# Performance work log

Hardware: AMD Instinct MI355X
Metric: run time of the kernel (lower is better)

The kernel has to match this reference:

```python
import jax, jax.numpy as jnp
import numpy as np

N_QUESTIONS = 2000
N_CATS = 4
MEMORY_SIZE = 50
KEY_DIM = 50
VALUE_DIM = 200
FINAL_FC = 50
ABILITY_SCALE = 3.0
BATCH = 1024
SEQ_LEN = 500


def setup_inputs() -> dict:
    key = jax.random.key(0)
    ks = jax.random.split(key, 20)
    f32 = jnp.float32
    inp = {}
    # integer data: question ids in [1, n_questions], responses in [0, K)
    inp['q_data'] = jax.random.randint(ks[0], (BATCH, SEQ_LEN), 1, N_QUESTIONS + 1)
    inp['r_data'] = jax.random.randint(ks[1], (BATCH, SEQ_LEN), 0, N_CATS)
    s = 0.05
    inp['q_embed_w'] = jax.random.normal(ks[2], (N_QUESTIONS + 1, KEY_DIM), f32) * s
    inp['Mk'] = jax.random.normal(ks[3], (MEMORY_SIZE, KEY_DIM), f32) * s
    inp['Mv0'] = jax.random.normal(ks[4], (MEMORY_SIZE, VALUE_DIM), f32) * s
    inp['Wv'] = jax.random.normal(ks[5], (VALUE_DIM, N_CATS * N_QUESTIONS), f32) * s
    inp['bv'] = jnp.zeros((VALUE_DIM,), f32)
    # DKVMN erase / add transforms
    inp['We'] = jax.random.normal(ks[6], (VALUE_DIM, VALUE_DIM), f32) * s
    inp['be'] = jnp.zeros((VALUE_DIM,), f32)
    inp['Wa'] = jax.random.normal(ks[7], (VALUE_DIM, VALUE_DIM), f32) * s
    inp['ba'] = jnp.zeros((VALUE_DIM,), f32)
    # summary network
    inp['Ws'] = jax.random.normal(ks[8], (FINAL_FC, VALUE_DIM + KEY_DIM), f32) * s
    inp['bs'] = jnp.zeros((FINAL_FC,), f32)
    # ability / threshold / discrimination heads
    inp['Wth'] = jax.random.normal(ks[9], (1, FINAL_FC), f32) * s
    inp['bth'] = jnp.zeros((1,), f32)
    inp['Wbeta'] = jax.random.normal(ks[10], (N_CATS - 1, KEY_DIM), f32) * s
    inp['bbeta'] = jnp.zeros((N_CATS - 1,), f32)
    inp['Wdisc'] = jax.random.normal(ks[11], (1, FINAL_FC + KEY_DIM), f32) * s
    inp['bdisc'] = jnp.zeros((1,), f32)
    return inp


def _deep_gpcm(q_data, r_data, q_embed_w, Mk, Mv0, Wv, bv, We, be, Wa, ba,
               Ws, bs, Wth, bth, Wbeta, bbeta, Wdisc, bdisc):
    B, S = q_data.shape
    K = Wbeta.shape[0] + 1
    D = Wv.shape[0]
    Q = Wv.shape[1] // K
    # view gpcm_value_embed weight as (D, K, Q): one-hot(q) @ W == gather column q
    WvK = Wv.reshape(D, K, Q)
    k_idx = jnp.arange(K, dtype=jnp.float32)
    Mv_init = jnp.broadcast_to(Mv0[None], (B,) + Mv0.shape)

    def step(Mv, inp):
        q_t, r_t = inp  # (B,), (B,)
        qe = q_embed_w[q_t]  # (B, key_dim)
        # linear decay weights: max(0, 1 - |k - r| / (K-1))
        w = jnp.maximum(0.0, 1.0 - jnp.abs(k_idx[None, :] - r_t[:, None].astype(jnp.float32)) / (K - 1))  # (B, K)
        Wvq = jnp.take(WvK, q_t - 1, axis=2)  # (D, K, B)
        ve = jnp.einsum('dkb,bk->bd', Wvq, w) + bv  # value embedding (B, D)
        # DKVMN attention + read
        cw = jax.nn.softmax(qe @ Mk.T, axis=-1)  # (B, mem)
        read = jnp.einsum('bm,bmd->bd', cw, Mv)
        # summary / IRT heads
        summary = jnp.tanh(jnp.concatenate([read, qe], axis=-1) @ Ws.T + bs)  # (B, fc)
        theta = ABILITY_SCALE * (summary @ Wth.T + bth)[:, 0]  # (B,)
        betas = jnp.tanh(qe @ Wbeta.T + bbeta)  # (B, K-1)
        alpha = jax.nn.softplus(jnp.concatenate([summary, qe], axis=-1) @ Wdisc.T + bdisc)[:, 0]  # (B,)
        # erase-add memory write
        erase = jax.nn.sigmoid(ve @ We.T + be)
        add = jnp.tanh(ve @ Wa.T + ba)
        Mv_new = Mv * (1.0 - cw[:, :, None] * erase[:, None, :]) + cw[:, :, None] * add[:, None, :]
        # GPCM cumulative logits -> softmax
        cum = jnp.cumsum(alpha[:, None] * (theta[:, None] - betas), axis=-1)  # (B, K-1)
        logits = jnp.concatenate([jnp.zeros((B, 1), cum.dtype), cum], axis=-1)  # (B, K)
        probs = jax.nn.softmax(logits, axis=-1)
        return Mv_new, probs

    _, probs = jax.lax.scan(step, Mv_init, (q_data.T, r_data.T))  # (S, B, K)
    return jnp.transpose(probs, (1, 0, 2))  # (B, S, K)


def reference(q_data, r_data, q_embed_w, Mk, Mv0, Wv, bv, We, be, Wa, ba,
              Ws, bs, Wth, bth, Wbeta, bbeta, Wdisc, bdisc):
    return _deep_gpcm(q_data, r_data, q_embed_w, Mk, Mv0, Wv, bv, We, be, Wa, ba,
                      Ws, bs, Wth, bth, Wbeta, bbeta, Wdisc, bdisc)
```

## Files before the change

kernel.cpp:

```cpp
#include <hip/hip_runtime.h>
#include <hip/hip_bf16.h>
#include <cstdint>
#include <cstddef>


namespace {
constexpr int kB   = 1024;
constexpr int kS   = 500;
constexpr int kQ   = 2000;
constexpr int kKD  = 50;
constexpr int kMem = 50;
constexpr int kD   = 200;
constexpr int kFC  = 50;
constexpr int kWP  = 216;

constexpr size_t OFF_EAD  = 0;
constexpr size_t OFF_CW   = OFF_EAD + (size_t)kQ * 4 * kD * 2;
constexpr size_t OFF_SQ   = OFF_CW + 100064;
constexpr size_t OFF_BQ   = OFF_SQ + 100064;
constexpr size_t OFF_DQ   = OFF_BQ + 8032;
constexpr size_t OFF_CE   = OFF_DQ + 2016;
constexpr size_t OFF_CA   = OFF_CE + 224;
constexpr size_t OFF_WET  = OFF_CA + 224;
constexpr size_t OFF_WAT  = OFF_WET + 40000;
}

typedef float f32x2 __attribute__((ext_vector_type(2)));
typedef _Float16 h2_t __attribute__((ext_vector_type(2)));

__device__ __forceinline__ f32x2 pk_fma(f32x2 a, f32x2 b, f32x2 c) {
  f32x2 d;
  asm("v_pk_fma_f32 %0, %1, %2, %3" : "=v"(d) : "v"(a), "v"(b), "v"(c));
  return d;
}

__device__ __forceinline__ void lds_barrier() {
  asm volatile("s_waitcnt lgkmcnt(0)" ::: "memory");
  __builtin_amdgcn_s_barrier();
  asm volatile("" ::: "memory");
}

__device__ __forceinline__ float fast_tanh(float x) {
  const float ax = fabsf(x);
  const float t = __expf(-2.f * ax);
  const float r = (1.f - t) / (1.f + t);
  return copysignf(r, x);
}
__device__ __forceinline__ float fast_softplus(float x) {
  return fmaxf(x, 0.f) + log1pf(__expf(-fabsf(x)));
}

__global__ void prep1_misc(const float* __restrict__ We, const float* __restrict__ Wa,
                           const float* __restrict__ bv, const float* __restrict__ be,
                           const float* __restrict__ ba, float* __restrict__ ws) {
  float* WeT = ws + OFF_WET;
  float* WaT = ws + OFF_WAT;
  float* ce  = ws + OFF_CE;
  float* ca  = ws + OFF_CA;
  const int gt = blockIdx.x * 256 + threadIdx.x;
  const int stride = gridDim.x * 256;
  for (int e = gt; e < kD * kD; e += stride) {
    const int i = e / kD;
    const int dd = e - i * kD;
    WeT[e] = We[dd * kD + i];
    WaT[e] = Wa[dd * kD + i];
  }
  for (int dd = gt; dd < kD; dd += stride) {
    float acc_e = be[dd], acc_a = ba[dd];
    for (int i = 0; i < kD; ++i) {
      acc_e = fmaf(We[dd * kD + i], bv[i], acc_e);
      acc_a = fmaf(Wa[dd * kD + i], bv[i], acc_a);
    }
    ce[dd] = acc_e;
    ca[dd] = acc_a;
  }
}

__global__ void prep2_ead(const float* __restrict__ Wv, float* __restrict__ ws) {
  __shared__ float s_wv[4][kD];
  const int tid = threadIdx.x;
  const int qm1 = blockIdx.x;
  for (int e = tid; e < 4 * kD; e += 256) {
    const int k = e / kD;
    const int i = e - k * kD;
    s_wv[k][i] = Wv[(size_t)i * (4 * kQ) + (size_t)k * kQ + qm1];
  }
  __syncthreads();
  const int d = tid;
  if (d < kD) {
    const float* WeT = ws + OFF_WET;
    const float* WaT = ws + OFF_WAT;
    float e0 = 0.f, e1 = 0.f, e2 = 0.f, e3 = 0.f;
    float a0 = 0.f, a1 = 0.f, a2 = 0.f, a3 = 0.f;
    for (int i = 0; i < kD; ++i) {
      const float we = WeT[i * kD + d];
      const float wa = WaT[i * kD + d];
      e0 = fmaf(we, s_wv[0][i], e0);
      e1 = fmaf(we, s_wv[1][i], e1);
      e2 = fmaf(we, s_wv[2][i], e2);
      e3 = fmaf(we, s_wv[3][i], e3);
      a0 = fmaf(wa, s_wv[0][i], a0);
      a1 = fmaf(wa, s_wv[1][i], a1);
      a2 = fmaf(wa, s_wv[2][i], a2);
      a3 = fmaf(wa, s_wv[3][i], a3);
    }
    const float ced = ws[OFF_CE + d];
    const float cad = ws[OFF_CA + d];
    const float W[4][4] = {{1.f, 2.f / 3.f, 1.f / 3.f, 0.f},
                           {2.f / 3.f, 1.f, 2.f / 3.f, 1.f / 3.f},
                           {1.f / 3.f, 2.f / 3.f, 1.f, 2.f / 3.f},
                           {0.f, 1.f / 3.f, 2.f / 3.f, 1.f}};
#pragma unroll
    for (int r = 0; r < 4; ++r) {
      const float ep = ced + W[r][0] * e0 + W[r][1] * e1 + W[r][2] * e2 + W[r][3] * e3;
      const float ap = cad + W[r][0] * a0 + W[r][1] * a1 + W[r][2] * a2 + W[r][3] * a3;
      float2 v;
      v.x = 1.f / (1.f + expf(-ep));
      v.y = tanhf(ap);
      *reinterpret_cast<float2*>(ws + OFF_EAD + ((size_t)(qm1 * 4 + r) * kD + d) * 2) = v;
    }
  }
}

__global__ void prep3_qtables(const float* __restrict__ q_embed_w, const float* __restrict__ Mk,
                              const float* __restrict__ Ws, const float* __restrict__ bs,
                              const float* __restrict__ Wbeta, const float* __restrict__ bbeta,
                              const float* __restrict__ Wdisc, float* __restrict__ ws) {
  __shared__ float s_qe[kKD];
  const int tid = threadIdx.x;
  const int q = blockIdx.x;
  if (tid < kKD) s_qe[tid] = q_embed_w[q * kKD + tid];
  __syncthreads();
  {
    float s = -1e30f;
    if (tid < kMem) {
      s = 0.f;
      for (int j = 0; j < kKD; ++j) s = fmaf(s_qe[j], Mk[tid * kKD + j], s);
    }
    float mx = s;
#pragma unroll
    for (int o = 1; o < 64; o <<= 1) mx = fmaxf(mx, __shfl_xor(mx, o));
    const float ev = (tid < kMem) ? expf(s - mx) : 0.f;
    float sm = ev;
#pragma unroll
    for (int o = 1; o < 64; o <<= 1) sm += __shfl_xor(sm, o);
    if (tid < kMem) ws[OFF_CW + (size_t)q * kMem + tid] = ev / sm;
  }
  if (tid < kFC) {
    float s = bs[tid];
    for (int j = 0; j < kKD; ++j) s = fmaf(s_qe[j], Ws[tid * 250 + kD + j], s);
    ws[OFF_SQ + (size_t)q * kFC + tid] = s;
  }
  if (tid < 4) {
    float v = 0.f;
    if (tid < 3) {
      float s = bbeta[tid];
      for (int j = 0; j < kKD; ++j) s = fmaf(s_qe[j], Wbeta[tid * kKD + j], s);
      v = tanhf(s);
    }
    ws[OFF_BQ + (size_t)q * 4 + tid] = v;
  }
  if (tid == 0) {
    float s = 0.f;
    for (int j = 0; j < kKD; ++j) s = fmaf(s_qe[j], Wdisc[kFC + j], s);
    ws[OFF_DQ + q] = s;
  }
}

__device__ __forceinline__ void do_finale(int l, float wth_f, float wds_f, float bth0,
                                          float bdisc0, const float (*s_part)[64],
                                          const float* s_sq_row, const float* s_bqdq_row,
                                          float* out_ptr) {
  float summ = 0.f;
  if (l < kFC) {
    const float sp = s_part[0][l] + s_part[1][l] + s_part[2][l] + s_part[3][l] +
                     s_part[4][l] + s_sq_row[l];
    summ = fast_tanh(sp);
  }
  float p1 = wth_f * summ;
  float p2 = wds_f * summ;
#pragma unroll
  for (int o = 1; o < 64; o <<= 1) {
    p1 += __shfl_xor(p1, o);
    p2 += __shfl_xor(p2, o);
  }
  if (l == 0) {
    const float theta = 3.f * (p1 + bth0);
    const float alpha = fast_softplus(p2 + s_bqdq_row[3] + bdisc0);
    const float c1 = alpha * (theta - s_bqdq_row[0]);
    const float c2 = c1 + alpha * (theta - s_bqdq_row[1]);
    const float c3 = c2 + alpha * (theta - s_bqdq_row[2]);
    const float mx = fmaxf(fmaxf(0.f, c1), fmaxf(c2, c3));
    const float x0 = __expf(0.f - mx);
    const float x1 = __expf(c1 - mx);
    const float x2 = __expf(c2 - mx);
    const float x3 = __expf(c3 - mx);
    const float inv = 1.f / (x0 + x1 + x2 + x3);
    float4 pr;
    pr.x = x0 * inv;
    pr.y = x1 * inv;
    pr.z = x2 * inv;
    pr.w = x3 * inv;
    *reinterpret_cast<float4*>(out_ptr) = pr;
  }
}

__launch_bounds__(256, 4)
__global__ void dkvmn_main(const int* __restrict__ q_data, const int* __restrict__ r_data,
                           const float* __restrict__ Mv0, const float* __restrict__ Ws,
                           const float* __restrict__ Wth, const float* __restrict__ bth,
                           const float* __restrict__ Wdisc, const float* __restrict__ bdisc,
                           const float* __restrict__ ws, float* __restrict__ out) {
  const int tid = threadIdx.x;
  const int b = blockIdx.x;
  const int lane = tid & 63;
  const int wid = tid >> 6;
  const float* EAD = ws + OFF_EAD;
  const float* CW = ws + OFF_CW;
  const float* SQ = ws + OFF_SQ;
  const float* BQ = ws + OFF_BQ;
  const float* DQ = ws + OFF_DQ;

  __shared__ __align__(16) _Float16 s_wsh[kFC * kWP];
  __shared__ __align__(16) _Float16 s_readh[2][208];
  __shared__ __align__(16) float s_cw[2][64];
  __shared__ float s_part[2][5][64];
  __shared__ float s_sq[3][52];
  __shared__ float s_bqdq[3][4];
  __shared__ int s_q[kS];
  __shared__ int s_qr[kS];

  for (int e = tid; e < kFC * kD; e += 256) {
    const int f = e / kD;
    const int dd = e - f * kD;
    s_wsh[f * kWP + dd] = (_Float16)Ws[f * 250 + dd];
  }
  {
    const int* qrow = q_data + (size_t)b * kS;
    const int* rrow = r_data + (size_t)b * kS;
    for (int e = tid; e < kS; e += 256) {
      const int qv = qrow[e];
      s_q[e] = qv;
      s_qr[e] = (qv - 1) * 4 + rrow[e];
    }
  }
  f32x2 mv[25];
  const int d = tid;
  const bool dact = (d < kD);
  if (dact) {
#pragma unroll
    for (int m = 0; m < 25; ++m) {
      mv[m][0] = Mv0[(2 * m) * kD + d];
      mv[m][1] = Mv0[(2 * m + 1) * kD + d];
    }
  }
  float wth_f = 0.f, wds_f = 0.f;
  if (wid == 3 && lane < kFC) {
    wth_f = Wth[lane];
    wds_f = Wdisc[lane];
  }
  const float bth0 = bth[0];
  const float bdisc0 = bdisc[0];
  float* out_b = out + (size_t)b * kS * 4;
  __syncthreads();

  const int q0 = s_q[0];
  const int q1 = s_q[1];
  float2 ea_cur = make_float2(0.f, 0.f);
  if (dact) ea_cur = *reinterpret_cast<const float2*>(EAD + ((size_t)s_qr[0] * kD + d) * 2);
  float cw_cur = 0.f;
  if (wid == 1 && lane < kMem) {
    s_cw[0][lane] = CW[(size_t)q0 * kMem + lane];
    cw_cur = CW[(size_t)q1 * kMem + lane];
  }
  float v2_cur = 0.f;
  if (wid == 2) {
    if (lane < kFC) v2_cur = SQ[(size_t)q0 * kFC + lane];
    else if (lane < 53) v2_cur = BQ[(size_t)q0 * 4 + (lane - 50)];
    else if (lane == 53) v2_cur = DQ[q0];
  }
  __syncthreads();

  int i3 = 0;
  for (int t = 0; t < kS; ++t) {
    const int pb = t & 1;
    const int ip1 = (i3 + 1 < 3) ? i3 + 1 : 0;
    const int tn1 = (t + 1 < kS) ? t + 1 : kS - 1;
    const int tn2 = (t + 2 < kS) ? t + 2 : kS - 1;
    f32x2 en2 = {0.f, 0.f}, ad2 = {0.f, 0.f};
    float2 ea_nxt = ea_cur;
    if (dact) {
      ea_nxt = *reinterpret_cast<const float2*>(EAD + ((size_t)s_qr[tn1] * kD + d) * 2);
      en2[0] = -ea_cur.x;
      en2[1] = -ea_cur.x;
      ad2[0] = ea_cur.y;
      ad2[1] = ea_cur.y;
    }
    if (wid == 1 && lane < kMem) {
      s_cw[pb ^ 1][lane] = cw_cur;
      cw_cur = CW[(size_t)s_q[tn2] * kMem + lane];
    }
    if (wid == 2) {
      const int qn = s_q[tn1];
      if (lane < kFC) {
        s_sq[i3][lane] = v2_cur;
        v2_cur = SQ[(size_t)qn * kFC + lane];
      } else if (lane < 53) {
        s_bqdq[i3][lane - 50] = v2_cur;
        v2_cur = BQ[(size_t)qn * 4 + (lane - 50)];
      } else if (lane == 53) {
        s_bqdq[i3][3] = v2_cur;
        v2_cur = DQ[qn];
      }
    }
    if (dact) {
      f32x2 r2a = {0.f, 0.f}, r2b = {0.f, 0.f};
      const float4* cw4 = reinterpret_cast<const float4*>(s_cw[pb]);
#pragma unroll
      for (int g = 0; g < 12; ++g) {
        const float4 c4 = cw4[g];
        const f32x2 clo = {c4.x, c4.y};
        const f32x2 chi = {c4.z, c4.w};
        r2a = pk_fma(clo, mv[2 * g], r2a);
        mv[2 * g] = pk_fma(clo, pk_fma(mv[2 * g], en2, ad2), mv[2 * g]);
        r2b = pk_fma(chi, mv[2 * g + 1], r2b);
        mv[2 * g + 1] = pk_fma(chi, pk_fma(mv[2 * g + 1], en2, ad2), mv[2 * g + 1]);
      }
      {
        const f32x2 clast = *reinterpret_cast<const f32x2*>(&s_cw[pb][48]);
        r2a = pk_fma(clast, mv[24], r2a);
        mv[24] = pk_fma(clast, pk_fma(mv[24], en2, ad2), mv[24]);
      }
      s_readh[pb][d] = (_Float16)((r2a[0] + r2b[0]) + (r2a[1] + r2b[1]));
    }
    if (wid == 3 && t >= 2) {
      do_finale(lane, wth_f, wds_f, bth0, bdisc0, s_part[pb ^ 1], s_sq[ip1], s_bqdq[ip1],
                out_b + (size_t)(t - 2) * 4);
    }
    if (tid < 250) {
      const int pc = tid / 50;
      const int pf = tid - pc * 50;
      const float4* wp = reinterpret_cast<const float4*>(s_wsh + pf * kWP + pc * 40);
      const float4* rp = reinterpret_cast<const float4*>(&s_readh[pb ^ 1][pc * 40]);
      float acc0 = 0.f, acc1 = 0.f;
#pragma unroll
      for (int g = 0; g < 5; ++g) {
        const float4 wv = wp[g];
        const float4 rv = rp[g];
        acc0 = __builtin_amdgcn_fdot2(__builtin_bit_cast(h2_t, wv.x),
                                      __builtin_bit_cast(h2_t, rv.x), acc0, false);
        acc1 = __builtin_amdgcn_fdot2(__builtin_bit_cast(h2_t, wv.y),
                                      __builtin_bit_cast(h2_t, rv.y), acc1, false);
        acc0 = __builtin_amdgcn_fdot2(__builtin_bit_cast(h2_t, wv.z),
                                      __builtin_bit_cast(h2_t, rv.z), acc0, false);
        acc1 = __builtin_amdgcn_fdot2(__builtin_bit_cast(h2_t, wv.w),
                                      __builtin_bit_cast(h2_t, rv.w), acc1, false);
      }
      s_part[pb][pc][pf] = acc0 + acc1;
    }
    lds_barrier();
    ea_cur = ea_nxt;
    i3 = ip1;
  }
  {
    constexpr int pbE = kS & 1;
    constexpr int i3a = (kS - 2) % 3;
    constexpr int i3b = (kS - 1) % 3;
    if (tid < 250) {
      const int pc = tid / 50;
      const int pf = tid - pc * 50;
      const float4* wp = reinterpret_cast<const float4*>(s_wsh + pf * kWP + pc * 40);
      const float4* rp = reinterpret_cast<const float4*>(&s_readh[(kS - 1) & 1][pc * 40]);
      float acc0 = 0.f, acc1 = 0.f;
#pragma unroll
      for (int g = 0; g < 5; ++g) {
        const float4 wv = wp[g];
        const float4 rv = rp[g];
        acc0 = __builtin_amdgcn_fdot2(__builtin_bit_cast(h2_t, wv.x),
                                      __builtin_bit_cast(h2_t, rv.x), acc0, false);
        acc1 = __builtin_amdgcn_fdot2(__builtin_bit_cast(h2_t, wv.y),
                                      __builtin_bit_cast(h2_t, rv.y), acc1, false);
        acc0 = __builtin_amdgcn_fdot2(__builtin_bit_cast(h2_t, wv.z),
                                      __builtin_bit_cast(h2_t, rv.z), acc0, false);
        acc1 = __builtin_amdgcn_fdot2(__builtin_bit_cast(h2_t, wv.w),
                                      __builtin_bit_cast(h2_t, rv.w), acc1, false);
      }
      s_part[pbE][pc][pf] = acc0 + acc1;
    }
    if (wid == 3) {
      do_finale(lane, wth_f, wds_f, bth0, bdisc0, s_part[pbE ^ 1], s_sq[i3a], s_bqdq[i3a],
                out_b + (size_t)(kS - 2) * 4);
    }
    lds_barrier();
    if (wid == 3) {
      do_finale(lane, wth_f, wds_f, bth0, bdisc0, s_part[pbE], s_sq[i3b], s_bqdq[i3b],
                out_b + (size_t)(kS - 1) * 4);
    }
  }
}

extern "C" void kernel_launch(void* const* d_in, const int* in_sizes, int n_in,
                              void* d_out, int out_size, void* d_ws, size_t ws_size,
                              hipStream_t stream) {
  (void)in_sizes; (void)n_in; (void)out_size; (void)ws_size;
  const int* q_data = (const int*)d_in[0];
  const int* r_data = (const int*)d_in[1];
  const float* q_embed_w = (const float*)d_in[2];
  const float* Mk = (const float*)d_in[3];
  const float* Mv0 = (const float*)d_in[4];
  const float* Wv = (const float*)d_in[5];
  const float* bv = (const float*)d_in[6];
  const float* We = (const float*)d_in[7];
  const float* be = (const float*)d_in[8];
  const float* Wa = (const float*)d_in[9];
  const float* ba = (const float*)d_in[10];
  const float* Ws = (const float*)d_in[11];
  const float* bs = (const float*)d_in[12];
  const float* Wth = (const float*)d_in[13];
  const float* bth = (const float*)d_in[14];
  const float* Wbeta = (const float*)d_in[15];
  const float* bbeta = (const float*)d_in[16];
  const float* Wdisc = (const float*)d_in[17];
  const float* bdisc = (const float*)d_in[18];
  float* out = (float*)d_out;
  float* ws = (float*)d_ws;

  hipLaunchKernelGGL(prep1_misc, dim3(64), dim3(256), 0, stream, We, Wa, bv, be, ba, ws);
  hipLaunchKernelGGL(prep2_ead, dim3(kQ), dim3(256), 0, stream, Wv, ws);
  hipLaunchKernelGGL(prep3_qtables, dim3(kQ + 1), dim3(64), 0, stream, q_embed_w, Mk, Ws, bs,
                     Wbeta, bbeta, Wdisc, ws);
  hipLaunchKernelGGL(dkvmn_main, dim3(kB), dim3(256), 0, stream, q_data, r_data, Mv0, Ws, Wth,
                     bth, Wdisc, bdisc, ws, out);
}
```

Baseline: 1.246 ms.

## Split memory-slot update across two threads per value column with 512-thread blocks

Doubles the block to 512 threads. The 50 memory slots of each value column are now split between two threads, which halves the per-thread serial FMA chain and the register footprint of the memory state. Load and finale roles move to warps 0 and 1. The Ws dot-product threads now add the two partial read vectors in fp16 before the fdot2. This adds thread-level parallelism in the sequential scan step, at the cost of an extra fp16 add (with some precision loss) and larger barrier groups.

```diff
diff --git a/kernel.cpp b/kernel.cpp
--- a/kernel.cpp
+++ b/kernel.cpp
@@ -205,7 +205,7 @@
   }
 }
 
-__launch_bounds__(256, 4)
+__launch_bounds__(512, 8)
 __global__ void dkvmn_main(const int* __restrict__ q_data, const int* __restrict__ r_data,
                            const float* __restrict__ Mv0, const float* __restrict__ Ws,
                            const float* __restrict__ Wth, const float* __restrict__ bth,
@@ -222,7 +222,7 @@
   const float* DQ = ws + OFF_DQ;
 
   __shared__ __align__(16) _Float16 s_wsh[kFC * kWP];
-  __shared__ __align__(16) _Float16 s_readh[2][208];
+  __shared__ __align__(16) _Float16 s_readh[2][2][208];
   __shared__ __align__(16) float s_cw[2][64];
   __shared__ float s_part[2][5][64];
   __shared__ float s_sq[3][52];
@@ -230,7 +230,7 @@
   __shared__ int s_q[kS];
   __shared__ int s_qr[kS];
 
-  for (int e = tid; e < kFC * kD; e += 256) {
+  for (int e = tid; e < kFC * kD; e += 512) {
     const int f = e / kD;
     const int dd = e - f * kD;
     s_wsh[f * kWP + dd] = (_Float16)Ws[f * 250 + dd];
@@ -238,24 +238,40 @@
   {
     const int* qrow = q_data + (size_t)b * kS;
     const int* rrow = r_data + (size_t)b * kS;
-    for (int e = tid; e < kS; e += 256) {
+    for (int e = tid; e < kS; e += 512) {
       const int qv = qrow[e];
       s_q[e] = qv;
       s_qr[e] = (qv - 1) * 4 + rrow[e];
     }
   }
-  f32x2 mv[25];
-  const int d = tid;
-  const bool dact = (d < kD);
+  const bool dact = (tid >= 112);
+  const int u = tid - 112;
+  const bool half1 = (u >= 200);
+  const int d = half1 ? (u - 200) : u;
+  const int p0 = half1 ? 13 : 0;
+
+  const bool pact = (tid >= 262);
+  const int pidx = tid - 262;
+  const int pc = pidx / 50;
+  const int pf = pidx - pc * 50;
+
+  f32x2 mv[13];
+#pragma unroll
+  for (int j = 0; j < 13; ++j) mv[j] = f32x2{0.f, 0.f};
   if (dact) {
 #pragma unroll
-    for (int m = 0; m < 25; ++m) {
-      mv[m][0] = Mv0[(2 * m) * kD + d];
-      mv[m][1] = Mv0[(2 * m + 1) * kD + d];
+    for (int j = 0; j < 12; ++j) {
+      const int m2 = 2 * (p0 + j);
+      mv[j][0] = Mv0[m2 * kD + d];
+      mv[j][1] = Mv0[(m2 + 1) * kD + d];
+    }
+    if (!half1) {
+      mv[12][0] = Mv0[24 * kD + d];
+      mv[12][1] = Mv0[25 * kD + d];
     }
   }
   float wth_f = 0.f, wds_f = 0.f;
-  if (wid == 3 && lane < kFC) {
+  if (wid == 0 && lane < kFC) {
     wth_f = Wth[lane];
     wds_f = Wdisc[lane];
   }
@@ -267,16 +283,16 @@
   const int q0 = s_q[0];
   const int q1 = s_q[1];
   float2 ea_cur = make_float2(0.f, 0.f);
-  if (dact) ea_cur = *reinterpret_cast<const float2*>(EAD + ((size_t)s_qr[0] * kD + d) * 2);
+  if (dact) ea_cur = *(reinterpret_cast<const float2*>(EAD) + (s_qr[0] * kD + d));
   float cw_cur = 0.f;
-  if (wid == 1 && lane < kMem) {
-    s_cw[0][lane] = CW[(size_t)q0 * kMem + lane];
-    cw_cur = CW[(size_t)q1 * kMem + lane];
+  if (wid == 0 && lane < kMem) {
+    s_cw[0][lane] = CW[q0 * kMem + lane];
+    cw_cur = CW[q1 * kMem + lane];
   }
   float v2_cur = 0.f;
-  if (wid == 2) {
-    if (lane < kFC) v2_cur = SQ[(size_t)q0 * kFC + lane];
-    else if (lane < 53) v2_cur = BQ[(size_t)q0 * 4 + (lane - 50)];
+  if (wid == 1) {
+    if (lane < kFC) v2_cur = SQ[q0 * kFC + lane];
+    else if (lane < 53) v2_cur = BQ[q0 * 4 + (lane - 50)];
     else if (lane == 53) v2_cur = DQ[q0];
   }
   __syncthreads();
@@ -290,24 +306,24 @@
     f32x2 en2 = {0.f, 0.f}, ad2 = {0.f, 0.f};
     float2 ea_nxt = ea_cur;
     if (dact) {
-      ea_nxt = *reinterpret_cast<const float2*>(EAD + ((size_t)s_qr[tn1] * kD + d) * 2);
+      ea_nxt = *(reinterpret_cast<const float2*>(EAD) + (s_qr[tn1] * kD + d));
       en2[0] = -ea_cur.x;
       en2[1] = -ea_cur.x;
       ad2[0] = ea_cur.y;
       ad2[1] = ea_cur.y;
     }
-    if (wid == 1 && lane < kMem) {
+    if (wid == 0 && lane < kMem) {
       s_cw[pb ^ 1][lane] = cw_cur;
-      cw_cur = CW[(size_t)s_q[tn2] * kMem + lane];
-    }
-    if (wid == 2) {
+      cw_cur = CW[s_q[tn2] * kMem + lane];
+    }
+    if (wid == 1) {
       const int qn = s_q[tn1];
       if (lane < kFC) {
         s_sq[i3][lane] = v2_cur;
-        v2_cur = SQ[(size_t)qn * kFC + lane];
+        v2_cur = SQ[qn * kFC + lane];
       } else if (lane < 53) {
         s_bqdq[i3][lane - 50] = v2_cur;
-        v2_cur = BQ[(size_t)qn * 4 + (lane - 50)];
+        v2_cur = BQ[qn * 4 + (lane - 50)];
       } else if (lane == 53) {
         s_bqdq[i3][3] = v2_cur;
         v2_cur = DQ[qn];
@@ -315,46 +331,46 @@
     }
     if (dact) {
       f32x2 r2a = {0.f, 0.f}, r2b = {0.f, 0.f};
-      const float4* cw4 = reinterpret_cast<const float4*>(s_cw[pb]);
-#pragma unroll
-      for (int g = 0; g < 12; ++g) {
-        const float4 c4 = cw4[g];
-        const f32x2 clo = {c4.x, c4.y};
-        const f32x2 chi = {c4.z, c4.w};
-        r2a = pk_fma(clo, mv[2 * g], r2a);
-        mv[2 * g] = pk_fma(clo, pk_fma(mv[2 * g], en2, ad2), mv[2 * g]);
-        r2b = pk_fma(chi, mv[2 * g + 1], r2b);
-        mv[2 * g + 1] = pk_fma(chi, pk_fma(mv[2 * g + 1], en2, ad2), mv[2 * g + 1]);
+      const f32x2* cw2 = reinterpret_cast<const f32x2*>(s_cw[pb]) + p0;
+#pragma unroll
+      for (int j = 0; j < 12; ++j) {
+        const f32x2 c2 = cw2[j];
+        if (j & 1) {
+          r2b = pk_fma(c2, mv[j], r2b);
+        } else {
+          r2a = pk_fma(c2, mv[j], r2a);
+        }
+        mv[j] = pk_fma(c2, pk_fma(mv[j], en2, ad2), mv[j]);
       }
-      {
-        const f32x2 clast = *reinterpret_cast<const f32x2*>(&s_cw[pb][48]);
-        r2a = pk_fma(clast, mv[24], r2a);
-        mv[24] = pk_fma(clast, pk_fma(mv[24], en2, ad2), mv[24]);
+      if (!half1) {
+        const f32x2 c2 = cw2[12];
+        r2a = pk_fma(c2, mv[12], r2a);
+        mv[12] = pk_fma(c2, pk_fma(mv[12], en2, ad2), mv[12]);
       }
-      s_readh[pb][d] = (_Float16)((r2a[0] + r2b[0]) + (r2a[1] + r2b[1]));
-    }
-    if (wid == 3 && t >= 2) {
+      s_readh[pb][half1][d] = (_Float16)((r2a[0] + r2b[0]) + (r2a[1] + r2b[1]));
+    }
+    if (wid == 0 && t >= 2) {
       do_finale(lane, wth_f, wds_f, bth0, bdisc0, s_part[pb ^ 1], s_sq[ip1], s_bqdq[ip1],
                 out_b + (size_t)(t - 2) * 4);
     }
-    if (tid < 250) {
-      const int pc = tid / 50;
-      const int pf = tid - pc * 50;
+    if (pact) {
       const float4* wp = reinterpret_cast<const float4*>(s_wsh + pf * kWP + pc * 40);
-      const float4* rp = reinterpret_cast<const float4*>(&s_readh[pb ^ 1][pc * 40]);
+      const float4* rpA = reinterpret_cast<const float4*>(&s_readh[pb ^ 1][0][pc * 40]);
+      const float4* rpB = reinterpret_cast<const float4*>(&s_readh[pb ^ 1][1][pc * 40]);
       float acc0 = 0.f, acc1 = 0.f;
 #pragma unroll
       for (int g = 0; g < 5; ++g) {
         const float4 wv = wp[g];
-        const float4 rv = rp[g];
-        acc0 = __builtin_amdgcn_fdot2(__builtin_bit_cast(h2_t, wv.x),
-                                      __builtin_bit_cast(h2_t, rv.x), acc0, false);
-        acc1 = __builtin_amdgcn_fdot2(__builtin_bit_cast(h2_t, wv.y),
-                                      __builtin_bit_cast(h2_t, rv.y), acc1, false);
-        acc0 = __builtin_amdgcn_fdot2(__builtin_bit_cast(h2_t, wv.z),
-                                      __builtin_bit_cast(h2_t, rv.z), acc0, false);
-        acc1 = __builtin_amdgcn_fdot2(__builtin_bit_cast(h2_t, wv.w),
-                                      __builtin_bit_cast(h2_t, rv.w), acc1, false);
+        const float4 va = rpA[g];
+        const float4 vb = rpB[g];
+        const h2_t r0 = __builtin_bit_cast(h2_t, va.x) + __builtin_bit_cast(h2_t, vb.x);
+        const h2_t r1 = __builtin_bit_cast(h2_t, va.y) + __builtin_bit_cast(h2_t, vb.y);
+        const h2_t r2 = __builtin_bit_cast(h2_t, va.z) + __builtin_bit_cast(h2_t, vb.z);
+        const h2_t r3 = __builtin_bit_cast(h2_t, va.w) + __builtin_bit_cast(h2_t, vb.w);
+        acc0 = __builtin_amdgcn_fdot2(__builtin_bit_cast(h2_t, wv.x), r0, acc0, false);
+        acc1 = __builtin_amdgcn_fdot2(__builtin_bit_cast(h2_t, wv.y), r1, acc1, false);
+        acc0 = __builtin_amdgcn_fdot2(__builtin_bit_cast(h2_t, wv.z), r2, acc0, false);
+        acc1 = __builtin_amdgcn_fdot2(__builtin_bit_cast(h2_t, wv.w), r3, acc1, false);
       }
       s_part[pb][pc][pf] = acc0 + acc1;
     }
@@ -366,33 +382,33 @@
     constexpr int pbE = kS & 1;
     constexpr int i3a = (kS - 2) % 3;
     constexpr int i3b = (kS - 1) % 3;
-    if (tid < 250) {
-      const int pc = tid / 50;
-      const int pf = tid - pc * 50;
+    if (pact) {
       const float4* wp = reinterpret_cast<const float4*>(s_wsh + pf * kWP + pc * 40);
-      const float4* rp = reinterpret_cast<const float4*>(&s_readh[(kS - 1) & 1][pc * 40]);
+      const float4* rpA = reinterpret_cast<const float4*>(&s_readh[(kS - 1) & 1][0][pc * 40]);
+      const float4* rpB = reinterpret_cast<const float4*>(&s_readh[(kS - 1) & 1][1][pc * 40]);
       float acc0 = 0.f, acc1 = 0.f;
 #pragma unroll
       for (int g = 0; g < 5; ++g) {
         const float4 wv = wp[g];
-        const float4 rv = rp[g];
-        acc0 = __builtin_amdgcn_fdot2(__builtin_bit_cast(h2_t, wv.x),
-                                      __builtin_bit_cast(h2_t, rv.x), acc0, false);
-        acc1 = __builtin_amdgcn_fdot2(__builtin_bit_cast(h2_t, wv.y),
-                                      __builtin_bit_cast(h2_t, rv.y), acc1, false);
-        acc0 = __builtin_amdgcn_fdot2(__builtin_bit_cast(h2_t, wv.z),
-                                      __builtin_bit_cast(h2_t, rv.z), acc0, false);
-        acc1 = __builtin_amdgcn_fdot2(__builtin_bit_cast(h2_t, wv.w),
-                                      __builtin_bit_cast(h2_t, rv.w), acc1, false);
+        const float4 va = rpA[g];
+        const float4 vb = rpB[g];
+        const h2_t r0 = __builtin_bit_cast(h2_t, va.x) + __builtin_bit_cast(h2_t, vb.x);
+        const h2_t r1 = __builtin_bit_cast(h2_t, va.y) + __builtin_bit_cast(h2_t, vb.y);
+        const h2_t r2 = __builtin_bit_cast(h2_t, va.z) + __builtin_bit_cast(h2_t, vb.z);
+        const h2_t r3 = __builtin_bit_cast(h2_t, va.w) + __builtin_bit_cast(h2_t, vb.w);
+        acc0 = __builtin_amdgcn_fdot2(__builtin_bit_cast(h2_t, wv.x), r0, acc0, false);
+        acc1 = __builtin_amdgcn_fdot2(__builtin_bit_cast(h2_t, wv.y), r1, acc1, false);
+        acc0 = __builtin_amdgcn_fdot2(__builtin_bit_cast(h2_t, wv.z), r2, acc0, false);
+        acc1 = __builtin_amdgcn_fdot2(__builtin_bit_cast(h2_t, wv.w), r3, acc1, false);
       }
       s_part[pbE][pc][pf] = acc0 + acc1;
     }
-    if (wid == 3) {
+    if (wid == 0) {
       do_finale(lane, wth_f, wds_f, bth0, bdisc0, s_part[pbE ^ 1], s_sq[i3a], s_bqdq[i3a],
                 out_b + (size_t)(kS - 2) * 4);
     }
     lds_barrier();
-    if (wid == 3) {
+    if (wid == 0) {
       do_finale(lane, wth_f, wds_f, bth0, bdisc0, s_part[pbE], s_sq[i3b], s_bqdq[i3b],
                 out_b + (size_t)(kS - 1) * 4);
     }
@@ -429,6 +445,6 @@
   hipLaunchKernelGGL(prep2_ead, dim3(kQ), dim3(256), 0, stream, Wv, ws);
   hipLaunchKernelGGL(prep3_qtables, dim3(kQ + 1), dim3(64), 0, stream, q_embed_w, Mk, Ws, bs,
                      Wbeta, bbeta, Wdisc, ws);
-  hipLaunchKernelGGL(dkvmn_main, dim3(kB), dim3(256), 0, stream, q_data, r_data, Mv0, Ws, Wth,
+  hipLaunchKernelGGL(dkvmn_main, dim3(kB), dim3(512), 0, stream, q_data, r_data, Mv0, Ws, Wth,
                      bth, Wdisc, bdisc, ws, out);
 }
```

Result: slower. 1.966 ms (+57.8%).
